# Performance work log

Measured on AMD Instinct MI355X. Metric: run time of the kernel, lower is better.

The kernel has to match this reference:

```python
import jax, jax.numpy as jnp
import numpy as np

B, C, H, W = 8, 256, 64, 64
DQK = 16  # int(sqrt(out_channels))


def setup_inputs() -> dict:
    key = jax.random.key(0)
    ks = jax.random.split(key, 8)
    s_in = 1.0 / np.sqrt(C)
    return {
        "x": jax.random.normal(ks[0], (B, C, H, W), dtype=jnp.float32),
        "Wf": jax.random.normal(ks[1], (DQK, C), dtype=jnp.float32) * s_in,
        "bf": jnp.zeros((DQK,), dtype=jnp.float32),
        "Wg": jax.random.normal(ks[2], (DQK, C), dtype=jnp.float32) * s_in,
        "bg": jnp.zeros((DQK,), dtype=jnp.float32),
        "Wh": jax.random.normal(ks[3], (C, C), dtype=jnp.float32) * s_in,
        "bh": jnp.zeros((C,), dtype=jnp.float32),
        # original inits attention_multiplier to 0.0; use small nonzero so output depends on attention path
        "gamma": jnp.float32(0.5),
    }


def reference(x, Wf, bf, Wg, bg, Wh, bh, gamma):
    b, c, h, w = x.shape
    hw = h * w
    # 1x1 convs == per-pixel channel projections
    f = (jnp.einsum('bchw,oc->bohw', x, Wf) + bf[None, :, None, None]).reshape(b, -1, hw)  # [B,DQK,HW]
    g = (jnp.einsum('bchw,oc->bohw', x, Wg) + bg[None, :, None, None]).reshape(b, -1, hw)  # [B,DQK,HW]
    hh = (jnp.einsum('bchw,oc->bohw', x, Wh) + bh[None, :, None, None]).reshape(b, -1, hw)  # [B,C,HW]
    # s[b,n,m] = sum_k g[b,k,n] * f[b,k,m]  -> [B,HW,HW]
    s = jnp.einsum('bkn,bkm->bnm', g, f)
    beta = jax.nn.softmax(s, axis=-1)
    # o = beta @ h^T, then transpose back to channel-first: [B,C,HW]
    o = jnp.einsum('bnm,bcm->bcn', beta, hh)
    return gamma * o.reshape(x.shape) + x
```

## Files before the change

kernel.cpp:

```cpp
#include <hip/hip_runtime.h>
#include <math.h>

#define BATCH 8
#define CH    256
#define HWN   4096
#define DQK   16

typedef __attribute__((ext_vector_type(8))) short short8;
typedef __attribute__((ext_vector_type(4))) float float4v;

__device__ __forceinline__ unsigned short f2bf(float f) {
    union { float f; unsigned int u; } v; v.f = f;
    unsigned int r = v.u + 0x7FFF + ((v.u >> 16) & 1);
    return (unsigned short)(r >> 16);
}
__device__ __forceinline__ unsigned int cvtpk(float lo, float hi) {
    unsigned int r;
    asm("v_cvt_pk_bf16_f32 %0, %1, %2" : "=v"(r) : "v"(lo), "v"(hi));
    return r;
}
__device__ __forceinline__ int perm_ft(int m) {
    return (m & ~28) | ((m & 24) >> 1) | ((m & 4) << 2);
}

__global__ __launch_bounds__(256) void wcast_kernel(
    const float* __restrict__ Wf, const float* __restrict__ bf_,
    const float* __restrict__ Wg, const float* __restrict__ bg,
    const float* __restrict__ Wh, const float* __restrict__ bh,
    unsigned short* __restrict__ Wbf, float* __restrict__ bcat)
{
    const int r = blockIdx.x;
    const int t = threadIdx.x;
    const float* src = (r < 16) ? (Wf + r*CH) : (r < 32) ? (Wg + (r-16)*CH) : (Wh + (r-32)*CH);
    Wbf[r*CH + t] = f2bf(src[t]);
    if (t == 0) bcat[r] = (r < 16) ? bf_[r] : (r < 32) ? bg[r-16] : bh[r-32];
}

__global__ __launch_bounds__(256) void xt_kernel(const float* __restrict__ x,
                                                 unsigned short* __restrict__ xt)
{
    const int t  = threadIdx.x;
    const int p0 = blockIdx.x * 64;
    const int c0 = blockIdx.y * 64;
    const int b  = blockIdx.z;
    __shared__ unsigned short tile[64][73];
    const int pc = t & 63;
    const int r0 = (t >> 6) * 16;
    #pragma unroll
    for (int j = 0; j < 16; j++) {
        int c = r0 + j;
        tile[pc][c] = f2bf(x[(size_t)(b*CH + c0 + c)*HWN + p0 + pc]);
    }
    __syncthreads();
    const int pr = t >> 2;
    const int cb = (t & 3) * 16;
    unsigned int outv[8];
    #pragma unroll
    for (int i = 0; i < 8; i++)
        outv[i] = (unsigned int)tile[pr][cb + 2*i] | ((unsigned int)tile[pr][cb + 2*i + 1] << 16);
    unsigned short* dst = &xt[(size_t)(b*HWN + p0 + pr)*CH + c0 + cb];
    *(uint4*)dst       = *(uint4*)&outv[0];
    *(uint4*)(dst + 8) = *(uint4*)&outv[4];
}

__global__ __launch_bounds__(256, 6) void proj_kernel(
    const unsigned short* __restrict__ xt, const unsigned short* __restrict__ Wbf,
    const float* __restrict__ bcat,
    unsigned short* __restrict__ ft, unsigned short* __restrict__ g,
    unsigned short* __restrict__ h3)
{
    const int t      = threadIdx.x;
    const int px0    = blockIdx.x * 64;
    const int b      = blockIdx.y;
    const int rtbase = blockIdx.z * 6;
    const int lane = t & 63, w = t >> 6, l15 = lane & 15, quad = lane >> 4;

    float4v acc[6];
    #pragma unroll
    for (int rt = 0; rt < 6; rt++) acc[rt] = (float4v){0.f,0.f,0.f,0.f};

    const unsigned short* xrow = &xt[((size_t)(b*HWN + px0 + w*16 + l15))*CH + quad*8];
    const unsigned short* wrow = &Wbf[(size_t)l15*CH + quad*8];

    #pragma unroll
    for (int ks = 0; ks < 8; ks++) {
        short8 afrag = *(const short8*)&xrow[ks*32];
        #pragma unroll
        for (int rt = 0; rt < 6; rt++) {
            short8 bfrag = *(const short8*)&wrow[(size_t)(rtbase + rt)*16*CH + ks*32];
            acc[rt] = __builtin_amdgcn_mfma_f32_16x16x32_bf16(afrag, bfrag, acc[rt], 0, 0, 0);
        }
    }

    const int pxl = px0 + w*16 + quad*4;
    const int mt  = (px0 >> 5) + (w >> 1);
    const int sub = ((w & 1)*2 + (quad >> 1))*128 + l15*8 + (quad & 1)*4;
    #pragma unroll
    for (int rt = 0; rt < 6; rt++) {
        const int R = rtbase + rt;
        if (R == 0) {
            float bv = bcat[l15];
            const int s0 = perm_ft(pxl);
            unsigned int p01 = cvtpk(acc[rt][0] + bv, acc[rt][1] + bv);
            unsigned int p23 = cvtpk(acc[rt][2] + bv, acc[rt][3] + bv);
            unsigned short* fp0 = &ft[((size_t)b*HWN + s0)*32];
            fp0[l15]       = (unsigned short)p01;         fp0[16 + l15]  = 0;
            fp0[32 + l15]  = (unsigned short)(p01 >> 16); fp0[48 + l15]  = 0;
            fp0[64 + l15]  = (unsigned short)p23;         fp0[80 + l15]  = 0;
            fp0[96 + l15]  = (unsigned short)(p23 >> 16); fp0[112 + l15] = 0;
        } else if (R == 1) {
            float bv = bcat[16 + l15];
            unsigned int a01 = cvtpk(acc[rt][0] + bv, acc[rt][1] + bv);
            unsigned int a23 = cvtpk(acc[rt][2] + bv, acc[rt][3] + bv);
            *(uint2*)&g[(size_t)(b*DQK + l15)*HWN + pxl] = make_uint2(a01, a23);
        } else {
            float bv = bcat[R*16 + l15];
            unsigned int u0 = cvtpk(acc[rt][0] + bv, acc[rt][1] + bv);
            unsigned int u1 = cvtpk(acc[rt][2] + bv, acc[rt][3] + bv);
            *(uint2*)&h3[(((size_t)((b*128 + mt)*16 + (R-2))) << 9) + sub] = make_uint2(u0, u1);
        }
    }
}

__global__ __launch_bounds__(512, 4) void attn_kernel(
    const unsigned short* __restrict__ ft, const unsigned short* __restrict__ g,
    const unsigned short* __restrict__ h3, const float* __restrict__ x,
    const float* __restrict__ gamma_p, float* __restrict__ out)
{
    const int t    = threadIdx.x;
    const int b    = blockIdx.x & 7;
    const int q0   = (blockIdx.x >> 3) * 64;
    const int lane = t & 63, w = t >> 6, l15 = lane & 15, quad = lane >> 4;
    const int qt_w = w >> 1, half = w & 1;

    __shared__ __align__(16) uint4 pB[2][2][4][64];
    __shared__ float l_l[4][16][2];

    union { short8 v; unsigned short u[8]; } gfrag;
    #pragma unroll
    for (int j = 0; j < 8; j++) {
        int k = quad*8 + j;
        gfrag.u[j] = (k < DQK) ? g[(size_t)(b*DQK + k)*HWN + q0 + qt_w*16 + l15] : (unsigned short)0;
    }

    const unsigned short* ftb = ft + (size_t)b*HWN*32;
    const unsigned short* h3b = h3 + ((size_t)b << 20);

    short8 fr[2][2], hr[2][2][2];
    float4v acc[2][4];
    #pragma unroll
    for (int i = 0; i < 2; i++)
        #pragma unroll
        for (int j = 0; j < 4; j++) acc[i][j] = (float4v){0.f,0.f,0.f,0.f};
    float l_acc = 0.f;
    uint4 P;

    #pragma unroll
    for (int j = 0; j < 2; j++)
        fr[0][j] = *(const short8*)&ftb[(size_t)((half*2 + j)*16 + l15)*32 + quad*8];
    {
        float4v z = {0.f,0.f,0.f,0.f};
        float4v s0v = __builtin_amdgcn_mfma_f32_16x16x32_bf16(fr[0][0], gfrag.v, z, 0, 0, 0);
        float4v s1v = __builtin_amdgcn_mfma_f32_16x16x32_bf16(fr[0][1], gfrag.v, z, 0, 0, 0);
        float e0 = __expf(s0v[0]), e1 = __expf(s0v[1]), e2 = __expf(s0v[2]), e3 = __expf(s0v[3]);
        float e4 = __expf(s1v[0]), e5 = __expf(s1v[1]), e6 = __expf(s1v[2]), e7 = __expf(s1v[3]);
        l_acc += (e0 + e1) + (e2 + e3) + (e4 + e5) + (e6 + e7);
        P = make_uint4(cvtpk(e0, e1), cvtpk(e2, e3), cvtpk(e4, e5), cvtpk(e6, e7));
    }
    #pragma unroll
    for (int j = 0; j < 2; j++)
        fr[1][j] = *(const short8*)&ftb[(size_t)(64 + (half*2 + j)*16 + l15)*32 + quad*8];
    #pragma unroll
    for (int grp = 0; grp < 2; grp++)
        #pragma unroll
        for (int ctl = 0; ctl < 2; ctl++)
            hr[0][grp][ctl] = *(const short8*)&h3b[(((size_t)(grp*16 + w*2 + ctl)) << 9) + lane*8];

#define ATTN_STEP(u, i, DO_NEXT) do {                                          \
    pB[u][half][qt_w][lane] = P;                                               \
    __syncthreads();                                                           \
    if (DO_NEXT) {                                                             \
      const int nf = ((i) + 2) & 63;                                           \
      _Pragma("unroll")                                                        \
      for (int j = 0; j < 2; j++)                                              \
        fr[u][j] = *(const short8*)&ftb[(size_t)(nf*64 + (half*2 + j)*16 + l15)*32 + quad*8]; \
      const int nh = ((i) + 1) & 63;                                           \
      _Pragma("unroll")                                                        \
      for (int grp = 0; grp < 2; grp++)                                        \
        _Pragma("unroll")                                                      \
        for (int ctl = 0; ctl < 2; ctl++)                                      \
          hr[(u)^1][grp][ctl] = *(const short8*)&h3b[(((size_t)((nh*2 + grp)*16 + w*2 + ctl)) << 9) + lane*8]; \
      float4v z = {0.f,0.f,0.f,0.f};                                           \
      float4v s0v = __builtin_amdgcn_mfma_f32_16x16x32_bf16(fr[(u)^1][0], gfrag.v, z, 0, 0, 0); \
      float4v s1v = __builtin_amdgcn_mfma_f32_16x16x32_bf16(fr[(u)^1][1], gfrag.v, z, 0, 0, 0); \
      float e0 = __expf(s0v[0]), e1 = __expf(s0v[1]), e2 = __expf(s0v[2]), e3 = __expf(s0v[3]); \
      float e4 = __expf(s1v[0]), e5 = __expf(s1v[1]), e6 = __expf(s1v[2]), e7 = __expf(s1v[3]); \
      l_acc += (e0 + e1) + (e2 + e3) + (e4 + e5) + (e6 + e7);                  \
      P = make_uint4(cvtpk(e0, e1), cvtpk(e2, e3), cvtpk(e4, e5), cvtpk(e6, e7)); \
    }                                                                          \
    _Pragma("unroll")                                                          \
    for (int grp = 0; grp < 2; grp++) {                                        \
      _Pragma("unroll")                                                        \
      for (int qt = 0; qt < 4; qt++) {                                         \
        union { uint4 uu; short8 v; } bq;                                      \
        bq.uu = pB[u][grp][qt][lane];                                          \
        _Pragma("unroll")                                                      \
        for (int ctl = 0; ctl < 2; ctl++)                                      \
          acc[ctl][qt] = __builtin_amdgcn_mfma_f32_16x16x32_bf16(hr[u][grp][ctl], bq.v, acc[ctl][qt], 0, 0, 0); \
      }                                                                        \
    }                                                                          \
  } while (0)

    for (int i0 = 0; i0 < 62; i0 += 2) {
        ATTN_STEP(0, i0, 1);
        ATTN_STEP(1, i0 + 1, 1);
    }
    ATTN_STEP(0, 62, 1);
    ATTN_STEP(1, 63, 0);
#undef ATTN_STEP

    l_acc += __shfl_xor(l_acc, 16, 64);
    l_acc += __shfl_xor(l_acc, 32, 64);
    if (quad == 0) l_l[qt_w][l15][half] = l_acc;
    __syncthreads();

    const float gamma = *gamma_p;
    float linv[4];
    #pragma unroll
    for (int qt = 0; qt < 4; qt++) linv[qt] = 1.f / (l_l[qt][l15][0] + l_l[qt][l15][1]);
    #pragma unroll
    for (int ctl = 0; ctl < 2; ctl++) {
        #pragma unroll
        for (int r = 0; r < 4; r++) {
            int c = w*32 + ctl*16 + quad*4 + r;
            size_t base = (size_t)(b*CH + c)*HWN + q0;
            #pragma unroll
            for (int qt = 0; qt < 4; qt++) {
                size_t o = base + qt*16 + l15;
                out[o] = gamma * acc[ctl][qt][r] * linv[qt] + x[o];
            }
        }
    }
}

extern "C" void kernel_launch(void* const* d_in, const int* in_sizes, int n_in,
                              void* d_out, int out_size, void* d_ws, size_t ws_size,
                              hipStream_t stream) {
    const float* x     = (const float*)d_in[0];
    const float* Wf    = (const float*)d_in[1];
    const float* bf_   = (const float*)d_in[2];
    const float* Wg    = (const float*)d_in[3];
    const float* bg    = (const float*)d_in[4];
    const float* Wh    = (const float*)d_in[5];
    const float* bh    = (const float*)d_in[6];
    const float* gamma = (const float*)d_in[7];
    float* out = (float*)d_out;

    unsigned short* xt   = (unsigned short*)d_ws;
    unsigned short* ftp  = xt  + (size_t)BATCH*HWN*CH;
    unsigned short* g    = ftp + (size_t)BATCH*HWN*32;
    unsigned short* h3   = g   + (size_t)BATCH*DQK*HWN;
    unsigned short* Wbf  = h3  + (size_t)BATCH*128*16*512;
    float*          bcat = (float*)(Wbf + 288*CH);

    wcast_kernel<<<dim3(288), 256, 0, stream>>>(Wf, bf_, Wg, bg, Wh, bh, Wbf, bcat);
    xt_kernel<<<dim3(HWN/64, CH/64, BATCH), 256, 0, stream>>>(x, xt);
    proj_kernel<<<dim3(HWN/64, BATCH, 3), 256, 0, stream>>>(xt, Wbf, bcat, ftp, g, h3);
    attn_kernel<<<dim3((HWN/64)*BATCH), 512, 0, stream>>>(ftp, g, h3, x, gamma, out);
}
```

Baseline: 217.3 us.

## Fold log2e into f projection, use exp2, vectorize transpose, prioritize MFMA

Scales the f projection by log2(e) before bf16 packing so the attention loop can use the native exp2 instead of __expf, removing a multiply per exponent. Rewrites the x transpose kernel to load float4 and use packed bf16 conversion, and reads LDS as 32-bit words. Raises wave priority around the PV MFMA block with s_setprio. Folding the scale before bf16 rounding slightly changes the rounding of the logits.

```diff
diff --git a/kernel.cpp b/kernel.cpp
--- a/kernel.cpp
+++ b/kernel.cpp
@@ -9,6 +9,8 @@
 typedef __attribute__((ext_vector_type(8))) short short8;
 typedef __attribute__((ext_vector_type(4))) float float4v;
 
+#define L2E 1.4426950408889634f
+
 __device__ __forceinline__ unsigned short f2bf(float f) {
     union { float f; unsigned int u; } v; v.f = f;
     unsigned int r = v.u + 0x7FFF + ((v.u >> 16) & 1);
@@ -18,6 +20,13 @@
     unsigned int r;
     asm("v_cvt_pk_bf16_f32 %0, %1, %2" : "=v"(r) : "v"(lo), "v"(hi));
     return r;
+}
+__device__ __forceinline__ float ex2(float x) {
+#if __has_builtin(__builtin_amdgcn_exp2f)
+    return __builtin_amdgcn_exp2f(x);
+#else
+    return exp2f(x);
+#endif
 }
 __device__ __forceinline__ int perm_ft(int m) {
     return (m & ~28) | ((m & 24) >> 1) | ((m & 4) << 2);
@@ -43,13 +52,18 @@
     const int p0 = blockIdx.x * 64;
     const int c0 = blockIdx.y * 64;
     const int b  = blockIdx.z;
-    __shared__ unsigned short tile[64][73];
-    const int pc = t & 63;
-    const int r0 = (t >> 6) * 16;
-    #pragma unroll
-    for (int j = 0; j < 16; j++) {
-        int c = r0 + j;
-        tile[pc][c] = f2bf(x[(size_t)(b*CH + c0 + c)*HWN + p0 + pc]);
+    __shared__ unsigned short tile[64][74];
+    const int col4 = (t & 15) * 4;
+    const int cr   = t >> 4;
+    #pragma unroll
+    for (int j = 0; j < 4; j++) {
+        int c = cr + j*16;
+        float4 v = *(const float4*)&x[(size_t)(b*CH + c0 + c)*HWN + p0 + col4];
+        unsigned int u01 = cvtpk(v.x, v.y), u23 = cvtpk(v.z, v.w);
+        tile[col4+0][c] = (unsigned short)u01;
+        tile[col4+1][c] = (unsigned short)(u01 >> 16);
+        tile[col4+2][c] = (unsigned short)u23;
+        tile[col4+3][c] = (unsigned short)(u23 >> 16);
     }
     __syncthreads();
     const int pr = t >> 2;
@@ -57,7 +71,7 @@
     unsigned int outv[8];
     #pragma unroll
     for (int i = 0; i < 8; i++)
-        outv[i] = (unsigned int)tile[pr][cb + 2*i] | ((unsigned int)tile[pr][cb + 2*i + 1] << 16);
+        outv[i] = *(const unsigned int*)&tile[pr][cb + 2*i];
     unsigned short* dst = &xt[(size_t)(b*HWN + p0 + pr)*CH + c0 + cb];
     *(uint4*)dst       = *(uint4*)&outv[0];
     *(uint4*)(dst + 8) = *(uint4*)&outv[4];
@@ -101,8 +115,8 @@
         if (R == 0) {
             float bv = bcat[l15];
             const int s0 = perm_ft(pxl);
-            unsigned int p01 = cvtpk(acc[rt][0] + bv, acc[rt][1] + bv);
-            unsigned int p23 = cvtpk(acc[rt][2] + bv, acc[rt][3] + bv);
+            unsigned int p01 = cvtpk((acc[rt][0] + bv)*L2E, (acc[rt][1] + bv)*L2E);
+            unsigned int p23 = cvtpk((acc[rt][2] + bv)*L2E, (acc[rt][3] + bv)*L2E);
             unsigned short* fp0 = &ft[((size_t)b*HWN + s0)*32];
             fp0[l15]       = (unsigned short)p01;         fp0[16 + l15]  = 0;
             fp0[32 + l15]  = (unsigned short)(p01 >> 16); fp0[48 + l15]  = 0;
@@ -162,8 +176,8 @@
         float4v z = {0.f,0.f,0.f,0.f};
         float4v s0v = __builtin_amdgcn_mfma_f32_16x16x32_bf16(fr[0][0], gfrag.v, z, 0, 0, 0);
         float4v s1v = __builtin_amdgcn_mfma_f32_16x16x32_bf16(fr[0][1], gfrag.v, z, 0, 0, 0);
-        float e0 = __expf(s0v[0]), e1 = __expf(s0v[1]), e2 = __expf(s0v[2]), e3 = __expf(s0v[3]);
-        float e4 = __expf(s1v[0]), e5 = __expf(s1v[1]), e6 = __expf(s1v[2]), e7 = __expf(s1v[3]);
+        float e0 = ex2(s0v[0]), e1 = ex2(s0v[1]), e2 = ex2(s0v[2]), e3 = ex2(s0v[3]);
+        float e4 = ex2(s1v[0]), e5 = ex2(s1v[1]), e6 = ex2(s1v[2]), e7 = ex2(s1v[3]);
         l_acc += (e0 + e1) + (e2 + e3) + (e4 + e5) + (e6 + e7);
         P = make_uint4(cvtpk(e0, e1), cvtpk(e2, e3), cvtpk(e4, e5), cvtpk(e6, e7));
     }
@@ -193,11 +207,12 @@
       float4v z = {0.f,0.f,0.f,0.f};                                           \
       float4v s0v = __builtin_amdgcn_mfma_f32_16x16x32_bf16(fr[(u)^1][0], gfrag.v, z, 0, 0, 0); \
       float4v s1v = __builtin_amdgcn_mfma_f32_16x16x32_bf16(fr[(u)^1][1], gfrag.v, z, 0, 0, 0); \
-      float e0 = __expf(s0v[0]), e1 = __expf(s0v[1]), e2 = __expf(s0v[2]), e3 = __expf(s0v[3]); \
-      float e4 = __expf(s1v[0]), e5 = __expf(s1v[1]), e6 = __expf(s1v[2]), e7 = __expf(s1v[3]); \
+      float e0 = ex2(s0v[0]), e1 = ex2(s0v[1]), e2 = ex2(s0v[2]), e3 = ex2(s0v[3]); \
+      float e4 = ex2(s1v[0]), e5 = ex2(s1v[1]), e6 = ex2(s1v[2]), e7 = ex2(s1v[3]); \
       l_acc += (e0 + e1) + (e2 + e3) + (e4 + e5) + (e6 + e7);                  \
       P = make_uint4(cvtpk(e0, e1), cvtpk(e2, e3), cvtpk(e4, e5), cvtpk(e6, e7)); \
     }                                                                          \
+    __builtin_amdgcn_s_setprio(1);                                             \
     _Pragma("unroll")                                                          \
     for (int grp = 0; grp < 2; grp++) {                                        \
       _Pragma("unroll")                                                        \
@@ -209,6 +224,7 @@
           acc[ctl][qt] = __builtin_amdgcn_mfma_f32_16x16x32_bf16(hr[u][grp][ctl], bq.v, acc[ctl][qt], 0, 0, 0); \
       }                                                                        \
     }                                                                          \
+    __builtin_amdgcn_s_setprio(0);                                             \
   } while (0)
 
     for (int i0 = 0; i0 < 62; i0 += 2) {
```

Result: no change. 215.1 us (-1.0%).
